# Performance work log

Measured on AMD Instinct MI355X. Metric: run time of the kernel, lower is better.

Reference implementation:

```python
import jax, jax.numpy as jnp
import numpy as np
import math


def setup_inputs() -> dict:
    key = jax.random.key(0)
    B, H, CL, QL = 16, 128, 2048, 256
    k0, k1, k2 = jax.random.split(key, 3)
    context = jax.random.normal(k0, (B, H, CL), dtype=jnp.float32)
    question = jax.random.normal(k1, (B, H, QL), dtype=jnp.float32)
    c_mask = jnp.ones((B, CL), dtype=jnp.int32)
    q_mask = jnp.ones((B, QL), dtype=jnp.int32)
    lim = math.sqrt(1.0 / H)
    w = jax.random.uniform(k2, (3 * H,), minval=-lim, maxval=lim, dtype=jnp.float32)
    return {"context": context, "question": question, "c_mask": c_mask, "q_mask": q_mask, "w": w}


def reference(context, question, c_mask, q_mask, w):
    # context: (B, H, c_len), question: (B, H, q_len), w: (3H,)
    H = context.shape[1]
    ctx = jnp.transpose(context, (0, 2, 1))   # (B, c_len, H)
    qry = jnp.transpose(question, (0, 2, 1))  # (B, q_len, H)
    wq, wc, wcq = w[:H], w[H:2 * H], w[2 * H:]
    # Trilinear similarity computed directly (no (B,c,q,3H) materialization):
    # s[b,i,j] = wq.q_j + wc.c_i + wcq.(c_i*q_j); torch layout after transpose is (B, c_len, q_len)
    s = (ctx @ wc)[:, :, None] + (qry @ wq)[:, None, :] + jnp.einsum('bch,bqh->bcq', ctx * wcq, qry)
    NEG = jnp.float32(-1e30)
    s1 = jax.nn.softmax(jnp.where(q_mask[:, None, :] > 0, s, NEG), axis=2)  # softmax over q
    s2 = jax.nn.softmax(jnp.where(c_mask[:, :, None] > 0, s, NEG), axis=1)  # softmax over c
    a = jnp.einsum('bcq,bqh->bch', s1, qry)          # context-to-query attention
    l = jnp.einsum('bcq,bkq->bck', s1, s2)           # s1 @ s2^T, (B, c_len, c_len)
    b = jnp.einsum('bck,bkh->bch', l, ctx)           # query-to-context attention
    out = jnp.concatenate([ctx, a, ctx * a, ctx * b], axis=2)  # (B, c_len, 4H)
    # drop_prob=0 -> dropout is identity
    return jnp.transpose(out, (0, 2, 1))  # (B, 4H, c_len)
```

## Files before the change

kernel.cpp:

```cpp
#include <hip/hip_runtime.h>

typedef short bf16x8 __attribute__((ext_vector_type(8)));
typedef float f32x16 __attribute__((ext_vector_type(16)));
typedef float f32x4  __attribute__((ext_vector_type(4)));

constexpr int B  = 16;
constexpr int H  = 128;
constexpr int CL = 2048;
constexpr int QL = 256;
constexpr int SPLITK5 = 4;
constexpr int K5SEG = CL / SPLITK5;
constexpr int PSTR = K5SEG + 8;
constexpr float SHIFT = 8.0f;

__device__ __forceinline__ unsigned short f2bf(float x) {
  unsigned u = __float_as_uint(x);
  u += 0x7fffu + ((u >> 16) & 1u);
  return (unsigned short)(u >> 16);
}
__device__ __forceinline__ float bf2f(unsigned short u) {
  return __uint_as_float((unsigned)u << 16);
}

template<int L, bool SCALE, bool WOUT>
__device__ __forceinline__ void ktrans_body(
    const float* __restrict__ src, const float* __restrict__ wbias,
    const float* __restrict__ wscale,
    unsigned short* __restrict__ dlin, unsigned short* __restrict__ dT,
    float* __restrict__ pbias, float* __restrict__ outg0,
    int bxl, int h1, int b, int tid,
    unsigned short (*T)[72], float (*P)[64]) {
  const int c0 = bxl * 64;
  const int hh = tid >> 4;
  const int cc4 = (tid & 15) * 4;
  float4 part = make_float4(0.f, 0.f, 0.f, 0.f);
  #pragma unroll
  for (int it = 0; it < 4; ++it) {
    const int hrow = it * 16 + hh;
    const int h = h1 * 64 + hrow;
    float4 v = *(const float4*)&src[((size_t)b * H + h) * L + c0 + cc4];
    const float wb = wbias[h];
    part.x = fmaf(v.x, wb, part.x); part.y = fmaf(v.y, wb, part.y);
    part.z = fmaf(v.z, wb, part.z); part.w = fmaf(v.w, wb, part.w);
    if (WOUT) {
      f32x4 t;
      t[0] = v.x; t[1] = v.y; t[2] = v.z; t[3] = v.w;
      __builtin_nontemporal_store(
          t, (f32x4*)&outg0[((size_t)b * 4 * H + h) * (size_t)CL + c0 + cc4]);
    }
    ushort4 o;
    o.x = f2bf(v.x); o.y = f2bf(v.y); o.z = f2bf(v.z); o.w = f2bf(v.w);
    *(ushort4*)&dlin[((size_t)b * H + h) * L + c0 + cc4] = o;
    ushort4 ot;
    if (SCALE) {
      const float ws = wscale[h];
      ot.x = f2bf(v.x * ws); ot.y = f2bf(v.y * ws);
      ot.z = f2bf(v.z * ws); ot.w = f2bf(v.w * ws);
    } else {
      ot = o;
    }
    *(ushort4*)&T[hrow][cc4] = ot;
  }
  *(float4*)&P[hh][cc4] = part;
  __syncthreads();
  if (tid < 64) {
    float sum = 0.f;
    #pragma unroll
    for (int i = 0; i < 16; ++i) sum += P[i][tid];
    pbias[(size_t)h1 * B * L + (size_t)b * L + c0 + tid] = sum;
  }
  #pragma unroll
  for (int it = 0; it < 4; ++it) {
    int lin = it * 256 + tid;
    int c = lin >> 4, hc = (lin & 15) * 4;
    ushort4 o;
    o.x = T[hc + 0][c]; o.y = T[hc + 1][c];
    o.z = T[hc + 2][c]; o.w = T[hc + 3][c];
    *(ushort4*)&dT[((size_t)b * L + c0 + c) * H + h1 * 64 + hc] = o;
  }
}

__global__ __launch_bounds__(256) void ktrans_all(
    const float* __restrict__ ctx, const float* __restrict__ qry,
    const float* __restrict__ w,
    unsigned short* __restrict__ ctx_bf, unsigned short* __restrict__ ctxwT,
    unsigned short* __restrict__ qry_bf, unsigned short* __restrict__ qryT,
    float* __restrict__ pct, float* __restrict__ pqt,
    float* __restrict__ out) {
  __shared__ unsigned short T[64][72];
  __shared__ float P[16][64];
  const int h1 = blockIdx.y, b = blockIdx.z, tid = threadIdx.x;
  const int bx = blockIdx.x;
  if (bx < CL / 64) {
    ktrans_body<CL, true, true>(ctx, w + H, w + 2 * H, ctx_bf, ctxwT, pct, out,
                                bx, h1, b, tid, T, P);
  } else {
    ktrans_body<QL, false, false>(qry, w, w, qry_bf, qryT, pqt, nullptr,
                                  bx - CL / 64, h1, b, tid, T, P);
  }
}

__global__ __launch_bounds__(256) void k5_fused(
    const unsigned short* __restrict__ ctxwT, const unsigned short* __restrict__ qryT,
    const unsigned short* __restrict__ ctxbf,
    const float* __restrict__ pct, const float* __restrict__ pqt,
    const int* __restrict__ cmask,
    unsigned short* __restrict__ tpart, float* __restrict__ Lpart) {
  __shared__ unsigned short P[32 * PSTR];
  const int wg = blockIdx.x;
  const int b = wg & (B - 1);
  const int seg = (wg >> 4) & (SPLITK5 - 1);
  const int q0 = (wg >> 6) * 32;
  const int cseg = seg * K5SEG;
  const int tid = threadIdx.x;
  const int w = tid >> 6, l = tid & 63;
  const int lr = l & 31, hi = l >> 5;

  const unsigned short* ap = qryT + ((size_t)b * QL + q0 + lr) * H + hi * 8;
  bf16x8 afr[8];
  #pragma unroll
  for (int k = 0; k < 8; ++k) afr[k] = *(const bf16x8*)(ap + k * 16);

  #pragma unroll
  for (int t4 = 0; t4 < 4; ++t4) {
    const int cl = w * 128 + t4 * 32 + lr;
    const int c = cseg + cl;
    const unsigned short* bp = ctxwT + ((size_t)b * CL + c) * H + hi * 8;
    f32x16 acc = {};
    #pragma unroll
    for (int k = 0; k < 8; ++k) {
      bf16x8 bfr = *(const bf16x8*)(bp + k * 16);
      acc = __builtin_amdgcn_mfma_f32_32x32x16_bf16(afr[k], bfr, acc, 0, 0, 0);
    }
    const float ct = pct[b * CL + c] + pct[B * CL + b * CL + c];
    const bool cm = cmask[b * CL + c] > 0;
    #pragma unroll
    for (int g = 0; g < 4; ++g) {
      const int ql = 4 * hi + 8 * g;
      const int qbase = q0 + ql;
      float4 qa = *(const float4*)&pqt[b * QL + qbase];
      float4 qb = *(const float4*)&pqt[B * QL + b * QL + qbase];
      const int key = (g & 3) << 3;
      const int cs = cl ^ key;
      P[(ql + 0) * PSTR + cs] = f2bf(cm ? __expf(acc[4*g+0] + ct + qa.x + qb.x - SHIFT) : 0.f);
      P[(ql + 1) * PSTR + cs] = f2bf(cm ? __expf(acc[4*g+1] + ct + qa.y + qb.y - SHIFT) : 0.f);
      P[(ql + 2) * PSTR + cs] = f2bf(cm ? __expf(acc[4*g+2] + ct + qa.z + qb.z - SHIFT) : 0.f);
      P[(ql + 3) * PSTR + cs] = f2bf(cm ? __expf(acc[4*g+3] + ct + qa.w + qb.w - SHIFT) : 0.f);
    }
  }
  __syncthreads();

  const int h0 = w * 32;
  const unsigned short* bp2 = ctxbf + ((size_t)b * H + h0 + lr) * CL + cseg + hi * 8;
  const int rkey = ((lr >> 3) & 3) << 3;
  f32x16 acc = {};
  #pragma unroll
  for (int kc = 0; kc < 32; ++kc) {
    bf16x8 af = *(const bf16x8*)&P[lr * PSTR + ((kc * 16 + hi * 8) ^ rkey)];
    bf16x8 bfr = *(const bf16x8*)(bp2 + kc * 16);
    acc = __builtin_amdgcn_mfma_f32_32x32x16_bf16(af, bfr, acc, 0, 0, 0);
  }
  unsigned short* tp = tpart + (size_t)(seg * B + b) * QL * H;
  #pragma unroll
  for (int r = 0; r < 16; ++r) {
    int qrow = (r & 3) + 8 * (r >> 2) + 4 * hi;
    tp[(size_t)(q0 + qrow) * H + h0 + lr] = f2bf(acc[r]);
  }

  {
    const int ql = tid >> 3, j = tid & 7;
    const unsigned short* pr = &P[ql * PSTR + j * 64];
    float s = 0.f;
    #pragma unroll
    for (int k = 0; k < 8; ++k) {
      bf16x8 v = *(const bf16x8*)(pr + k * 8);
      #pragma unroll
      for (int i = 0; i < 8; ++i) s += bf2f((unsigned short)v[i]);
    }
    s += __shfl_xor(s, 1);
    s += __shfl_xor(s, 2);
    s += __shfl_xor(s, 4);
    if (j == 0) Lpart[((size_t)b * SPLITK5 + seg) * QL + q0 + ql] = s;
  }
}

__global__ __launch_bounds__(256) void k5b_treduce(
    const unsigned short* __restrict__ tpart, const float* __restrict__ Lpart,
    unsigned short* __restrict__ tTbf) {
  __shared__ unsigned short lds[16 * 66];
  __shared__ float cinv_s[64];
  const int q0 = blockIdx.x * 64, h0 = blockIdx.y * 16, b = blockIdx.z;
  const int tid = threadIdx.x;
  if (tid < 64) {
    float Ls = 0.f;
    #pragma unroll
    for (int s = 0; s < SPLITK5; ++s)
      Ls += Lpart[((size_t)b * SPLITK5 + s) * QL + q0 + tid];
    cinv_s[tid] = 1.0f / Ls;
  }
  __syncthreads();
  for (int lin = tid; lin < 64 * 16; lin += 256) {
    int q = lin >> 4, h = lin & 15;
    float v = 0.f;
    #pragma unroll
    for (int sgt = 0; sgt < SPLITK5; ++sgt)
      v += bf2f(tpart[((size_t)(sgt * B + b) * QL + q0 + q) * H + h0 + h]);
    lds[h * 66 + q] = f2bf(v * cinv_s[q]);
  }
  __syncthreads();
  for (int lin = tid; lin < 16 * 64; lin += 256) {
    int h = lin >> 6, q = lin & 63;
    tTbf[((size_t)b * H + h0 + h) * QL + q0 + q] = lds[h * 66 + q];
  }
}

__device__ __forceinline__ int qswz(int q, int c) {
  return q ^ (((c >> 3) & 7) << 3);
}

__global__ __launch_bounds__(256) void kb_fused(
    const unsigned short* __restrict__ ctxwT, const unsigned short* __restrict__ qryT,
    const unsigned short* __restrict__ qrybf, const unsigned short* __restrict__ tTbf,
    const unsigned short* __restrict__ ctxbf,
    const float* __restrict__ pct, const float* __restrict__ pqt,
    const int* __restrict__ qmask, float* __restrict__ out) {
  __shared__ unsigned short Ps[32 * 264];
  __shared__ float stats[32][4];
  const int wg = blockIdx.x;
  const int b = wg & (B - 1);
  const int c0 = (wg >> 4) * 32;
  const int tid = threadIdx.x;
  const int w = tid >> 6, l = tid & 63;
  const int lr = l & 31, hi = l >> 5;
  const int c = c0 + lr;

  const unsigned short* bp = ctxwT + ((size_t)b * CL + c) * H + hi * 8;
  bf16x8 bfr[8];
  #pragma unroll
  for (int k = 0; k < 8; ++k) bfr[k] = *(const bf16x8*)(bp + k * 16);

  const float ct = pct[b * CL + c] + pct[B * CL + b * CL + c];

  float rs = 0.f;
  #pragma unroll
  for (int t2 = 0; t2 < 2; ++t2) {
    const int q0 = (2 * w + t2) * 32;
    const unsigned short* ap = qryT + ((size_t)b * QL + q0 + lr) * H + hi * 8;
    f32x16 acc = {};
    #pragma unroll
    for (int k = 0; k < 8; ++k)
      acc = __builtin_amdgcn_mfma_f32_32x32x16_bf16(
          *(const bf16x8*)(ap + k * 16), bfr[k], acc, 0, 0, 0);
    #pragma unroll
    for (int g = 0; g < 4; ++g) {
      const int qbase = q0 + 4 * hi + 8 * g;
      float4 qa = *(const float4*)&pqt[b * QL + qbase];
      float4 qb = *(const float4*)&pqt[B * QL + b * QL + qbase];
      int4 m4 = *(const int4*)&qmask[b * QL + qbase];
      float e0 = m4.x > 0 ? __expf(acc[4*g+0] + ct + qa.x + qb.x - SHIFT) : 0.f;
      float e1 = m4.y > 0 ? __expf(acc[4*g+1] + ct + qa.y + qb.y - SHIFT) : 0.f;
      float e2 = m4.z > 0 ? __expf(acc[4*g+2] + ct + qa.z + qb.z - SHIFT) : 0.f;
      float e3 = m4.w > 0 ? __expf(acc[4*g+3] + ct + qa.w + qb.w - SHIFT) : 0.f;
      rs += e0 + e1 + e2 + e3;
      const unsigned v01 = (unsigned)f2bf(e0) | ((unsigned)f2bf(e1) << 16);
      const unsigned v23 = (unsigned)f2bf(e2) | ((unsigned)f2bf(e3) << 16);
      *(unsigned*)&Ps[lr * 264 + qswz(qbase, lr)] = v01;
      *(unsigned*)&Ps[lr * 264 + qswz(qbase + 2, lr)] = v23;
    }
  }
  rs += __shfl_xor(rs, 32);
  if (hi == 0) stats[lr][w] = rs;

  const int h0 = w * 32;
  unsigned short cvu[16];
  {
    const unsigned short* cvp = ctxbf + (size_t)b * H * CL + c;
    #pragma unroll
    for (int r = 0; r < 16; ++r) {
      const int h = h0 + (r & 3) + 8 * (r >> 2) + 4 * hi;
      cvu[r] = cvp[(size_t)h * CL];
    }
  }
  __syncthreads();
  const float rinv = 1.0f / (stats[lr][0] + stats[lr][1] + stats[lr][2] + stats[lr][3]);

  const unsigned short* a1p = qrybf + ((size_t)b * H + h0 + lr) * QL + hi * 8;
  const unsigned short* a2p = tTbf + ((size_t)b * H + h0 + lr) * QL + hi * 8;
  f32x16 accA = {}, accB = {};
  #pragma unroll
  for (int kc = 0; kc < 16; ++kc) {
    bf16x8 pb = *(const bf16x8*)&Ps[lr * 264 + qswz(kc * 16 + hi * 8, lr)];
    bf16x8 a1 = *(const bf16x8*)(a1p + kc * 16);
    bf16x8 a2 = *(const bf16x8*)(a2p + kc * 16);
    accA = __builtin_amdgcn_mfma_f32_32x32x16_bf16(a1, pb, accA, 0, 0, 0);
    accB = __builtin_amdgcn_mfma_f32_32x32x16_bf16(a2, pb, accB, 0, 0, 0);
  }
  float* ob = out + (size_t)b * 4 * H * CL;
  #pragma unroll
  for (int r = 0; r < 16; ++r) {
    const int h = h0 + (r & 3) + 8 * (r >> 2) + 4 * hi;
    const float cv = bf2f(cvu[r]);
    const float av = accA[r] * rinv;
    const float bv = accB[r] * rinv;
    __builtin_nontemporal_store(av, &ob[(size_t)(H + h) * CL + c]);
    __builtin_nontemporal_store(cv * av, &ob[(size_t)(2 * H + h) * CL + c]);
    __builtin_nontemporal_store(cv * bv, &ob[(size_t)(3 * H + h) * CL + c]);
  }
}

extern "C" void kernel_launch(void* const* d_in, const int* in_sizes, int n_in,
                              void* d_out, int out_size, void* d_ws, size_t ws_size,
                              hipStream_t stream) {
  const float* context  = (const float*)d_in[0];
  const float* question = (const float*)d_in[1];
  const int*   c_mask   = (const int*)d_in[2];
  const int*   q_mask   = (const int*)d_in[3];
  const float* w        = (const float*)d_in[4];
  float* out = (float*)d_out;

  char* ws = (char*)d_ws;
  size_t off = 0;
  auto alloc = [&](size_t bytes) -> void* {
    void* p = ws + off;
    off += (bytes + 255) & ~(size_t)255;
    return p;
  };
  unsigned short* ctx_bf = (unsigned short*)alloc((size_t)B * H * CL * 2);
  unsigned short* ctxwT  = (unsigned short*)alloc((size_t)B * CL * H * 2);
  unsigned short* qry_bf = (unsigned short*)alloc((size_t)B * H * QL * 2);
  unsigned short* qryT   = (unsigned short*)alloc((size_t)B * QL * H * 2);
  unsigned short* tpart  = (unsigned short*)alloc((size_t)SPLITK5 * B * QL * H * 2);
  unsigned short* tT_bf  = (unsigned short*)alloc((size_t)B * H * QL * 2);
  float* pct   = (float*)alloc((size_t)2 * B * CL * sizeof(float));
  float* pqt   = (float*)alloc((size_t)2 * B * QL * sizeof(float));
  float* Lpart = (float*)alloc((size_t)B * SPLITK5 * QL * sizeof(float));

  ktrans_all<<<dim3(CL / 64 + QL / 64, H / 64, B), dim3(256), 0, stream>>>(
      context, question, w, ctx_bf, ctxwT, qry_bf, qryT, pct, pqt, out);

  k5_fused<<<dim3((QL / 32) * SPLITK5 * B), dim3(256), 0, stream>>>(
      ctxwT, qryT, ctx_bf, pct, pqt, c_mask, tpart, Lpart);

  k5b_treduce<<<dim3(QL / 64, H / 16, B), dim3(256), 0, stream>>>(
      tpart, Lpart, tT_bf);

  kb_fused<<<dim3((CL / 32) * B), dim3(256), 0, stream>>>(
      ctxwT, qryT, qry_bf, tT_bf, ctx_bf, pct, pqt, q_mask, out);
}
```

Baseline: 76.77 us.

## Split kb_fused across eight waves with split-K LDS reduction

Raises the final fused kernel from 4 to 8 waves per block. Each wave now computes one 32-wide q tile of the score/exp stage instead of two. The second GEMM stage is split over K, with the upper four waves summing their partial accumulators into the lower four through shared memory, which reuses the P buffer region. This adds per-wave parallelism and latency hiding, at the cost of an extra LDS reduction, two more barriers, and only half the waves doing the output stores.

```diff
diff --git a/kernel.cpp b/kernel.cpp
--- a/kernel.cpp
+++ b/kernel.cpp
@@ -218,14 +218,16 @@
   return q ^ (((c >> 3) & 7) << 3);
 }
 
-__global__ __launch_bounds__(256) void kb_fused(
+__global__ __launch_bounds__(512) void kb_fused8(
     const unsigned short* __restrict__ ctxwT, const unsigned short* __restrict__ qryT,
     const unsigned short* __restrict__ qrybf, const unsigned short* __restrict__ tTbf,
     const unsigned short* __restrict__ ctxbf,
     const float* __restrict__ pct, const float* __restrict__ pqt,
     const int* __restrict__ qmask, float* __restrict__ out) {
-  __shared__ unsigned short Ps[32 * 264];
-  __shared__ float stats[32][4];
+  __shared__ char smem[32768];
+  __shared__ float stats[32][8];
+  unsigned short* Ps = (unsigned short*)smem;
+  float* red = (float*)smem;
   const int wg = blockIdx.x;
   const int b = wg & (B - 1);
   const int c0 = (wg >> 4) * 32;
@@ -242,9 +244,8 @@
   const float ct = pct[b * CL + c] + pct[B * CL + b * CL + c];
 
   float rs = 0.f;
-  #pragma unroll
-  for (int t2 = 0; t2 < 2; ++t2) {
-    const int q0 = (2 * w + t2) * 32;
+  {
+    const int q0 = w * 32;
     const unsigned short* ap = qryT + ((size_t)b * QL + q0 + lr) * H + hi * 8;
     f32x16 acc = {};
     #pragma unroll
@@ -271,9 +272,10 @@
   rs += __shfl_xor(rs, 32);
   if (hi == 0) stats[lr][w] = rs;
 
-  const int h0 = w * 32;
+  const int ht = w & 3;
+  const int h0 = ht * 32;
   unsigned short cvu[16];
-  {
+  if (w < 4) {
     const unsigned short* cvp = ctxbf + (size_t)b * H * CL + c;
     #pragma unroll
     for (int r = 0; r < 16; ++r) {
@@ -282,29 +284,54 @@
     }
   }
   __syncthreads();
-  const float rinv = 1.0f / (stats[lr][0] + stats[lr][1] + stats[lr][2] + stats[lr][3]);
-
+
+  const int kcb = (w >> 2) * 8;
   const unsigned short* a1p = qrybf + ((size_t)b * H + h0 + lr) * QL + hi * 8;
   const unsigned short* a2p = tTbf + ((size_t)b * H + h0 + lr) * QL + hi * 8;
   f32x16 accA = {}, accB = {};
   #pragma unroll
-  for (int kc = 0; kc < 16; ++kc) {
+  for (int j = 0; j < 8; ++j) {
+    const int kc = kcb + j;
     bf16x8 pb = *(const bf16x8*)&Ps[lr * 264 + qswz(kc * 16 + hi * 8, lr)];
     bf16x8 a1 = *(const bf16x8*)(a1p + kc * 16);
     bf16x8 a2 = *(const bf16x8*)(a2p + kc * 16);
     accA = __builtin_amdgcn_mfma_f32_32x32x16_bf16(a1, pb, accA, 0, 0, 0);
     accB = __builtin_amdgcn_mfma_f32_32x32x16_bf16(a2, pb, accB, 0, 0, 0);
   }
-  float* ob = out + (size_t)b * 4 * H * CL;
-  #pragma unroll
-  for (int r = 0; r < 16; ++r) {
-    const int h = h0 + (r & 3) + 8 * (r >> 2) + 4 * hi;
-    const float cv = bf2f(cvu[r]);
-    const float av = accA[r] * rinv;
-    const float bv = accB[r] * rinv;
-    __builtin_nontemporal_store(av, &ob[(size_t)(H + h) * CL + c]);
-    __builtin_nontemporal_store(cv * av, &ob[(size_t)(2 * H + h) * CL + c]);
-    __builtin_nontemporal_store(cv * bv, &ob[(size_t)(3 * H + h) * CL + c]);
+  __syncthreads();
+
+  if (w >= 4) {
+    float* ra = &red[((ht * 2 + 0) * 16) * 64 + l];
+    float* rb = &red[((ht * 2 + 1) * 16) * 64 + l];
+    #pragma unroll
+    for (int r = 0; r < 16; ++r) {
+      ra[r * 64] = accA[r];
+      rb[r * 64] = accB[r];
+    }
+  }
+  __syncthreads();
+
+  if (w < 4) {
+    const float* ra = &red[((ht * 2 + 0) * 16) * 64 + l];
+    const float* rb = &red[((ht * 2 + 1) * 16) * 64 + l];
+    #pragma unroll
+    for (int r = 0; r < 16; ++r) {
+      accA[r] += ra[r * 64];
+      accB[r] += rb[r * 64];
+    }
+    const float rinv = 1.0f / (stats[lr][0] + stats[lr][1] + stats[lr][2] + stats[lr][3] +
+                               stats[lr][4] + stats[lr][5] + stats[lr][6] + stats[lr][7]);
+    float* ob = out + (size_t)b * 4 * H * CL;
+    #pragma unroll
+    for (int r = 0; r < 16; ++r) {
+      const int h = h0 + (r & 3) + 8 * (r >> 2) + 4 * hi;
+      const float cv = bf2f(cvu[r]);
+      const float av = accA[r] * rinv;
+      const float bv = accB[r] * rinv;
+      __builtin_nontemporal_store(av, &ob[(size_t)(H + h) * CL + c]);
+      __builtin_nontemporal_store(cv * av, &ob[(size_t)(2 * H + h) * CL + c]);
+      __builtin_nontemporal_store(cv * bv, &ob[(size_t)(3 * H + h) * CL + c]);
+    }
   }
 }
 
@@ -344,6 +371,6 @@
   k5b_treduce<<<dim3(QL / 64, H / 16, B), dim3(256), 0, stream>>>(
       tpart, Lpart, tT_bf);
 
-  kb_fused<<<dim3((CL / 32) * B), dim3(256), 0, stream>>>(
+  kb_fused8<<<dim3((CL / 32) * B), dim3(512), 0, stream>>>(
       ctxwT, qryT, qry_bf, tT_bf, ctx_bf, pct, pqt, q_mask, out);
 }
```

Measured after the change: 80.86 us. +5.3%, slower.
